# Kernel optimization log

Measured on AMD Instinct MI355X. Metric: run time of the kernel, lower is better.

## Reference

```python
import jax, jax.numpy as jnp
import numpy as np

ALPHA = 0.2  # tf.nn.leaky_relu default alpha
B, LATENT, T, N = 8, 256, 128, 768
F, L, E = 4, 3, 12288


def _causal_conv1d(x, w, b):
    # x: [B,T,Cin], w: [K,Cin,Cout] -> causal pad left by K-1
    k = w.shape[0]
    y = jax.lax.conv_general_dilated(x, w, (1,), ((k - 1, 0),),
                                     dimension_numbers=('NWC', 'WIO', 'NWC'))
    return y + b


def _same_conv1d(x, w, b):
    y = jax.lax.conv_general_dilated(x, w, (1,), 'SAME',
                                     dimension_numbers=('NWC', 'WIO', 'NWC'))
    return y + b


def _same_conv2d(x, w, b):
    y = jax.lax.conv_general_dilated(x, w, (1, 1), 'SAME',
                                     dimension_numbers=('NHWC', 'HWIO', 'NHWC'))
    return y + b


def _gat(nodes, row, col, qw, qb, kw, kb, vw, vb):
    # tf_geometric-style single-head GAT; row/col already contain self-loops.
    M = nodes.shape[0]
    Q = jax.nn.leaky_relu(nodes @ qw + qb, ALPHA)
    K = jax.nn.leaky_relu(nodes @ kw + kb, ALPHA)
    V = nodes @ vw
    scale = jnp.sqrt(jnp.asarray(Q.shape[-1], nodes.dtype))
    score = jnp.sum(Q[row] * K[col], axis=-1) / scale  # [E']
    smax = jax.ops.segment_max(score, row, num_segments=M)
    ex = jnp.exp(score - smax[row])
    den = jax.ops.segment_sum(ex, row, num_segments=M)
    att = ex / den[row]
    out = jax.ops.segment_sum(V[col] * att[:, None], row, num_segments=M)
    return out + vb


def _gw_layer(y, row, col, wa, ba, wb, bb, qw, qb, kw, kb, vw, vb, rw, rb):
    b_, t_, n_, f_ = y.shape
    x = jnp.moveaxis(y, -1, 0)  # [F,B,T,N]

    def branch(xf, wa_, ba_, wb_, bb_, qw_, qb_, kw_, kb_, vw_, vb_):
        a = jax.nn.sigmoid(_causal_conv1d(xf, wa_, ba_))
        g = a * jnp.tanh(_causal_conv1d(xf, wb_, bb_))   # gated TCN [B,T,N]
        nodes = g.transpose(0, 2, 1).reshape(b_ * n_, t_)  # node id = b*N + n
        h = _gat(nodes, row, col, qw_, qb_, kw_, kb_, vw_, vb_)
        return h.reshape(b_, n_, t_).transpose(0, 2, 1)  # [B,T,N]

    outs = jax.vmap(branch)(x, wa, ba, wb, bb, qw, qb, kw, kb, vw, vb)
    outs = jnp.moveaxis(outs, 0, -1)                      # [B,T,N,F]
    res = jnp.einsum('btnf,fg->btng', y, rw) + rb         # 1x1 res conv
    return outs + res


def _decoder(x, edges, shunt_dense_w, shunt_dense_b, shunt_c1_w, shunt_c1_b,
             shunt_c2_w, shunt_c2_b, tcn_a_w, tcn_a_b, tcn_b_w, tcn_b_b,
             gat_q_w, gat_q_b, gat_k_w, gat_k_b, gat_v_w, gat_v_b,
             res_w, res_b, skip_w, skip_b, out1_w, out1_b, out2_w, out2_b):
    # ConvShunt: [B,latent] -> [B,T] -> [B,T,N] -> [B,T,N,F]
    y = x @ shunt_dense_w + shunt_dense_b
    y = _same_conv1d(y[..., None], shunt_c1_w, shunt_c1_b)
    y = _same_conv2d(y[..., None], shunt_c2_w, shunt_c2_b)
    M = B * N
    self_idx = jnp.arange(M, dtype=edges.dtype)
    row = jnp.concatenate([edges[0], self_idx])
    col = jnp.concatenate([edges[1], self_idx])
    skips = []
    for i in range(L):
        y = _gw_layer(y, row, col, tcn_a_w[i], tcn_a_b[i], tcn_b_w[i], tcn_b_b[i],
                      gat_q_w[i], gat_q_b[i], gat_k_w[i], gat_k_b[i],
                      gat_v_w[i], gat_v_b[i], res_w[i], res_b[i])
        skips.append(jax.nn.leaky_relu(
            jnp.einsum('btnf,f->btn', y, skip_w[i]) + skip_b[i], ALPHA))
    s = jnp.stack(skips, axis=-1)                         # [B,T,N,L]
    g = jax.nn.leaky_relu(_same_conv2d(s, out1_w, out1_b), ALPHA)
    return _same_conv2d(g, out2_w, out2_b)                # [B,T,N,1]


def setup_inputs() -> dict:
    ks = iter(jax.random.split(jax.random.key(0), 32))

    def w(shape, fan_in):
        return jax.random.normal(next(ks), shape, jnp.float32) / np.sqrt(fan_in).astype(np.float32)

    return {
        'x': jax.random.normal(next(ks), (B, LATENT), jnp.float32),
        'edges': jax.random.randint(next(ks), (2, E), 0, N, jnp.int32),
        'shunt_dense_w': w((LATENT, T), LATENT),
        'shunt_dense_b': jnp.zeros((T,), jnp.float32),
        'shunt_c1_w': w((3, 1, N), 3),
        'shunt_c1_b': jnp.zeros((N,), jnp.float32),
        'shunt_c2_w': w((3, 3, 1, F), 9),
        'shunt_c2_b': jnp.zeros((F,), jnp.float32),
        'tcn_a_w': w((L, F, 5, N, N), 5 * N),
        'tcn_a_b': jnp.zeros((L, F, N), jnp.float32),
        'tcn_b_w': w((L, F, 5, N, N), 5 * N),
        'tcn_b_b': jnp.zeros((L, F, N), jnp.float32),
        'gat_q_w': w((L, F, T, T), T),
        'gat_q_b': jnp.zeros((L, F, T), jnp.float32),
        'gat_k_w': w((L, F, T, T), T),
        'gat_k_b': jnp.zeros((L, F, T), jnp.float32),
        'gat_v_w': w((L, F, T, T), T),
        'gat_v_b': jnp.zeros((L, F, T), jnp.float32),
        'res_w': w((L, F, F), F),
        'res_b': jnp.zeros((L, F), jnp.float32),
        'skip_w': w((L, F), F),
        'skip_b': jnp.zeros((L,), jnp.float32),
        'out1_w': w((3, 3, L, 1), 9 * L),
        'out1_b': jnp.zeros((1,), jnp.float32),
        'out2_w': w((1, 1, 1, 1), 1),
        'out2_b': jnp.zeros((1,), jnp.float32),
    }


def reference(x, edges, shunt_dense_w, shunt_dense_b, shunt_c1_w, shunt_c1_b,
              shunt_c2_w, shunt_c2_b, tcn_a_w, tcn_a_b, tcn_b_w, tcn_b_b,
              gat_q_w, gat_q_b, gat_k_w, gat_k_b, gat_v_w, gat_v_b,
              res_w, res_b, skip_w, skip_b, out1_w, out1_b, out2_w, out2_b):
    return _decoder(x, edges, shunt_dense_w, shunt_dense_b, shunt_c1_w, shunt_c1_b,
                    shunt_c2_w, shunt_c2_b, tcn_a_w, tcn_a_b, tcn_b_w, tcn_b_b,
                    gat_q_w, gat_q_b, gat_k_w, gat_k_b, gat_v_w, gat_v_b,
                    res_w, res_b, skip_w, skip_b, out1_w, out1_b, out2_w, out2_b)
```

## Files before the change

### kernel.cpp

```cpp
#include <hip/hip_runtime.h>
#include <math.h>

#define ALPHA_ 0.2f
#define AS1 __attribute__((address_space(1)))
#define AS3 __attribute__((address_space(3)))

constexpr int B_ = 8, LATENT_ = 256, T_ = 128, N_ = 768, F_ = 4, L_ = 3, E_ = 12288;
constexpr int M_ = B_ * N_;
constexpr int MT_ = B_ * T_;
constexpr int EP_ = E_ + M_;
constexpr int BTN_ = B_ * T_ * N_;
constexpr size_t SZ_ = (size_t)BTN_ * F_;
constexpr int KTCN_ = 5 * N_;
constexpr int KSPLIT_ = KTCN_ / 2;
constexpr int TP_ = T_ + 4;

typedef __bf16 bf16x8 __attribute__((ext_vector_type(8)));
typedef float f32x4 __attribute__((ext_vector_type(4)));

__device__ __forceinline__ float lrelu(float x) { return x > 0.0f ? x : ALPHA_ * x; }
__device__ __forceinline__ unsigned short f2bf(float x) {
    union { __bf16 h; unsigned short u; } c; c.h = (__bf16)x; return c.u;
}
__device__ __forceinline__ float bf2f(unsigned short u) {
    return __uint_as_float(((unsigned)u) << 16);
}

__global__ void k_dense(const float* __restrict__ x, const float* __restrict__ w,
                        const float* __restrict__ b, float* __restrict__ y0) {
    int i = blockIdx.x * blockDim.x + threadIdx.x;
    if (i >= B_ * T_) return;
    int bb = i / T_, t = i % T_;
    float acc = b[t];
    for (int l = 0; l < LATENT_; ++l) acc += x[bb * LATENT_ + l] * w[l * T_ + t];
    y0[i] = acc;
}

__global__ void k_conv1(const float* __restrict__ y0, const float* __restrict__ w,
                        const float* __restrict__ b, float* __restrict__ y1) {
    int i = blockIdx.x * blockDim.x + threadIdx.x;
    if (i >= BTN_) return;
    int n = i % N_, t = (i / N_) % T_, bb = i / (N_ * T_);
    float acc = b[n];
    #pragma unroll
    for (int k = 0; k < 3; ++k) {
        int tt = t - 1 + k;
        if (tt >= 0 && tt < T_) acc += y0[bb * T_ + tt] * w[k * N_ + n];
    }
    y1[i] = acc;
}

__global__ void k_conv2w(const float* __restrict__ y1, const float* __restrict__ w,
                         const float* __restrict__ b, float* __restrict__ y,
                         unsigned short* __restrict__ xTpad) {
    int i = blockIdx.x * blockDim.x + threadIdx.x;
    if (i >= BTN_) return;
    int n = i % N_, t = (i / N_) % T_, bb = i / (N_ * T_);
    float acc[F_];
    #pragma unroll
    for (int f = 0; f < F_; ++f) acc[f] = b[f];
    #pragma unroll
    for (int dt = 0; dt < 3; ++dt) {
        int tt = t - 1 + dt;
        if (tt < 0 || tt >= T_) continue;
        #pragma unroll
        for (int dn = 0; dn < 3; ++dn) {
            int nn = n - 1 + dn;
            if (nn < 0 || nn >= N_) continue;
            float v = y1[(bb * T_ + tt) * N_ + nn];
            #pragma unroll
            for (int f = 0; f < F_; ++f) acc[f] += v * w[(dt * 3 + dn) * F_ + f];
        }
    }
    #pragma unroll
    for (int f = 0; f < F_; ++f) {
        y[(size_t)i * F_ + f] = acc[f];
        xTpad[((size_t)(f * B_ + bb) * TP_ + 4 + t) * N_ + n] = f2bf(acc[f]);
    }
}

__global__ __launch_bounds__(256) void k_convT(const float* __restrict__ in,
        unsigned short* __restrict__ outT, int Kd, int Nd) {
    __shared__ float tl[32][33];
    const int f = blockIdx.z;
    in += (size_t)f * Kd * Nd;
    outT += (size_t)f * Kd * Nd;
    const int x0 = blockIdx.x * 32;
    const int y0 = blockIdx.y * 32;
    const int tx = threadIdx.x & 31, ty = threadIdx.x >> 5;
    #pragma unroll
    for (int r = 0; r < 4; ++r)
        tl[ty + r * 8][tx] = in[(size_t)(y0 + ty + r * 8) * Nd + x0 + tx];
    __syncthreads();
    #pragma unroll
    for (int r = 0; r < 4; ++r)
        outT[(size_t)(x0 + ty + r * 8) * Kd + y0 + tx] = f2bf(tl[tx][ty + r * 8]);
}

__global__ __launch_bounds__(256) void k_convT2(const float* __restrict__ in0,
        const float* __restrict__ in1, unsigned short* __restrict__ out0,
        unsigned short* __restrict__ out1) {
    __shared__ float tl[64][33];
    const int z = blockIdx.z;
    const int f = z & 3, wsel = z >> 2;
    const float* in = (wsel ? in1 : in0) + (size_t)f * KTCN_ * N_;
    unsigned short* outT = (wsel ? out1 : out0) + (size_t)f * KTCN_ * N_;
    const int n0 = blockIdx.x * 32, k0 = blockIdx.y * 64;
    const int tx = threadIdx.x & 31, ty = threadIdx.x >> 5;
    #pragma unroll
    for (int r = 0; r < 8; ++r)
        tl[ty + r * 8][tx] = in[(size_t)(k0 + ty + r * 8) * N_ + n0 + tx];
    __syncthreads();
    const int kx2 = threadIdx.x & 63, ny = threadIdx.x >> 6;
    #pragma unroll
    for (int r = 0; r < 8; ++r)
        outT[(size_t)(n0 + ny + r * 4) * KTCN_ + k0 + kx2] = f2bf(tl[kx2][ny + r * 4]);
}

__global__ __launch_bounds__(256) void k_tcn_mfma(
        const unsigned short* __restrict__ xTpad,
        const unsigned short* __restrict__ wat, const unsigned short* __restrict__ wbt,
        const float* __restrict__ ba, const float* __restrict__ bbias,
        float* __restrict__ oa0, float* __restrict__ oa1,
        float* __restrict__ ob0, float* __restrict__ ob1) {
    __shared__ unsigned short As[128 * 32];
    __shared__ unsigned short Bs[128 * 32];
    const int bid = blockIdx.x;
    const int bt = bid / 96;
    const int c = bid - bt * 96;
    const int xb = c % 6;
    const int zz = c / 6;
    const int f = zz & 3;
    const int wsel = (zz >> 2) & 1;
    const int s = zz >> 3;
    const int n0 = xb * 128;
    const unsigned short* xf = xTpad + (size_t)(f * B_ + bt) * TP_ * N_;
    const unsigned short* wf = (wsel ? wbt : wat) + (size_t)f * N_ * KTCN_ + (size_t)n0 * KTCN_;
    const float* bias = (wsel ? bbias : ba) + f * N_;
    float* out = (wsel ? (s ? ob1 : ob0) : (s ? oa1 : oa0));
    const int tid = threadIdx.x;
    const int lane = tid & 63;
    const int w = tid >> 6;
    const int wm = (w >> 1) * 64, wn = (w & 1) * 64;
    const int r16 = lane & 15, kb = lane >> 4;
    const int srow = lane >> 2;
    const int scol = (((lane & 3) ^ ((lane >> 3) & 3)) * 8);
    const int kx = (kb ^ ((r16 >> 1) & 3)) * 8;
    f32x4 acc[4][4] = {};
    const int k_lo = s * KSPLIT_, k_hi = k_lo + KSPLIT_;
    for (int kk0 = k_lo; kk0 < k_hi; kk0 += 32) {
        const int ks = kk0 / N_;
        const int nin0 = kk0 - ks * N_;
        #pragma unroll
        for (int h = 0; h < 2; ++h) {
            const int seg = w + 4 * h;
            const int row = seg * 16 + srow;
            const unsigned short* gA = xf + (size_t)(row + ks) * N_ + nin0 + scol;
            const unsigned short* gB = wf + (size_t)row * KTCN_ + kk0 + scol;
            __builtin_amdgcn_global_load_lds((const AS1 unsigned int*)(const void*)gA,
                    (AS3 unsigned int*)(void*)(As + seg * 512), 16, 0, 0);
            __builtin_amdgcn_global_load_lds((const AS1 unsigned int*)(const void*)gB,
                    (AS3 unsigned int*)(void*)(Bs + seg * 512), 16, 0, 0);
        }
        __syncthreads();
        bf16x8 av[4], bv[4];
        #pragma unroll
        for (int i = 0; i < 4; ++i) av[i] = *(const bf16x8*)(As + (wm + i * 16 + r16) * 32 + kx);
        #pragma unroll
        for (int j = 0; j < 4; ++j) bv[j] = *(const bf16x8*)(Bs + (wn + j * 16 + r16) * 32 + kx);
        #pragma unroll
        for (int i = 0; i < 4; ++i)
            #pragma unroll
            for (int j = 0; j < 4; ++j)
                acc[i][j] = __builtin_amdgcn_mfma_f32_16x16x32_bf16(av[i], bv[j], acc[i][j], 0, 0, 0);
        __syncthreads();
    }
    float* of = out + (size_t)(f * B_ + bt) * T_ * N_;
    #pragma unroll
    for (int i = 0; i < 4; ++i) {
        #pragma unroll
        for (int j = 0; j < 4; ++j) {
            const int n = n0 + wn + j * 16 + r16;
            const float bv2 = (s == 0) ? bias[n] : 0.0f;
            #pragma unroll
            for (int r = 0; r < 4; ++r) {
                const int m = wm + i * 16 + kb * 4 + r;
                of[(size_t)m * N_ + n] = acc[i][j][r] + bv2;
            }
        }
    }
}

__global__ __launch_bounds__(256) void k_gate_nodes(const float* __restrict__ a0,
        const float* __restrict__ a1, const float* __restrict__ b0,
        const float* __restrict__ b1, unsigned short* __restrict__ nodes) {
    __shared__ float tl[32][33];
    const int bz = blockIdx.z;
    const int t0 = blockIdx.x * 32, n0 = blockIdx.y * 32;
    const int tx = threadIdx.x & 31, ty = threadIdx.x >> 5;
    const size_t base = (size_t)bz * T_ * N_;
    #pragma unroll
    for (int r = 0; r < 4; ++r) {
        const size_t idx = base + (size_t)(t0 + ty + r * 8) * N_ + n0 + tx;
        const float av = a0[idx] + a1[idx], bvv = b0[idx] + b1[idx];
        tl[ty + r * 8][tx] = (1.0f / (1.0f + __expf(-av))) * tanhf(bvv);
    }
    __syncthreads();
    #pragma unroll
    for (int r = 0; r < 4; ++r)
        nodes[base + (size_t)(n0 + ty + r * 8) * T_ + t0 + tx] = f2bf(tl[tx][ty + r * 8]);
}

__global__ __launch_bounds__(256) void k_proj_mfma(
        const unsigned short* __restrict__ nodes, const unsigned short* __restrict__ pwt,
        const float* __restrict__ qb, const float* __restrict__ kbias,
        unsigned short* __restrict__ Q, unsigned short* __restrict__ K,
        unsigned short* __restrict__ V) {
    __shared__ unsigned short As[128 * 32];
    __shared__ unsigned short Bs[128 * 32];
    const int zz = blockIdx.z;
    const int f = zz & 3;
    const int sel = zz >> 2;
    const int m0 = blockIdx.y * 128;
    const unsigned short* af = nodes + (size_t)f * M_ * T_;
    const unsigned short* wfp = pwt + (size_t)sel * F_ * T_ * T_ + (size_t)f * T_ * T_;
    const float* bias = (sel == 0) ? qb : (sel == 1 ? kbias : nullptr);
    unsigned short* out = (sel == 0) ? Q : (sel == 1 ? K : V);
    const int tid = threadIdx.x;
    const int lane = tid & 63;
    const int w = tid >> 6;
    const int wm = (w >> 1) * 64, wn = (w & 1) * 64;
    const int r16 = lane & 15, kb = lane >> 4;
    const int srow = lane >> 2;
    const int scol = (((lane & 3) ^ ((lane >> 3) & 3)) * 8);
    const int kx = (kb ^ ((r16 >> 1) & 3)) * 8;
    f32x4 acc[4][4] = {};
    for (int kk0 = 0; kk0 < T_; kk0 += 32) {
        #pragma unroll
        for (int h = 0; h < 2; ++h) {
            const int seg = w + 4 * h;
            const int row = seg * 16 + srow;
            const unsigned short* gA = af + (size_t)(m0 + row) * T_ + kk0 + scol;
            const unsigned short* gB = wfp + (size_t)row * T_ + kk0 + scol;
            __builtin_amdgcn_global_load_lds((const AS1 unsigned int*)(const void*)gA,
                    (AS3 unsigned int*)(void*)(As + seg * 512), 16, 0, 0);
            __builtin_amdgcn_global_load_lds((const AS1 unsigned int*)(const void*)gB,
                    (AS3 unsigned int*)(void*)(Bs + seg * 512), 16, 0, 0);
        }
        __syncthreads();
        bf16x8 av[4], bv[4];
        #pragma unroll
        for (int i = 0; i < 4; ++i) av[i] = *(const bf16x8*)(As + (wm + i * 16 + r16) * 32 + kx);
        #pragma unroll
        for (int j = 0; j < 4; ++j) bv[j] = *(const bf16x8*)(Bs + (wn + j * 16 + r16) * 32 + kx);
        #pragma unroll
        for (int i = 0; i < 4; ++i)
            #pragma unroll
            for (int j = 0; j < 4; ++j)
                acc[i][j] = __builtin_amdgcn_mfma_f32_16x16x32_bf16(av[i], bv[j], acc[i][j], 0, 0, 0);
        __syncthreads();
    }
    const int do_l = (sel < 2);
    unsigned short* of = out + (size_t)f * M_ * T_;
    #pragma unroll
    for (int i = 0; i < 4; ++i) {
        #pragma unroll
        for (int j = 0; j < 4; ++j) {
            const int n = wn + j * 16 + r16;
            #pragma unroll
            for (int r = 0; r < 4; ++r) {
                const int m = m0 + wm + i * 16 + kb * 4 + r;
                float v = acc[i][j][r];
                if (bias) v += bias[f * T_ + n];
                if (do_l) v = lrelu(v);
                of[(size_t)m * T_ + n] = f2bf(v);
            }
        }
    }
}

__device__ __forceinline__ int edge_row(const int* e, int i) { return i < E_ ? e[i] : i - E_; }
__device__ __forceinline__ int edge_col(const int* e, int i) { return i < E_ ? e[E_ + i] : i - E_; }

__global__ void k_hist(const int* __restrict__ edges, int* __restrict__ deg) {
    int i = blockIdx.x * blockDim.x + threadIdx.x;
    if (i >= EP_) return;
    atomicAdd(&deg[edge_row(edges, i)], 1);
}

__global__ __launch_bounds__(256) void k_scan(const int* __restrict__ deg,
        int* __restrict__ rowptr, int* __restrict__ cursor) {
    __shared__ int part[256];
    const int tid = threadIdx.x;
    constexpr int PER = M_ / 256;
    int loc[PER];
    int s = 0;
    #pragma unroll
    for (int j = 0; j < PER; ++j) { loc[j] = s; s += deg[tid * PER + j]; }
    part[tid] = s;
    __syncthreads();
    if (tid == 0) {
        int run = 0;
        for (int i2 = 0; i2 < 256; ++i2) { int v = part[i2]; part[i2] = run; run += v; }
        rowptr[M_] = run;
    }
    __syncthreads();
    const int off = part[tid];
    #pragma unroll
    for (int j = 0; j < PER; ++j) {
        rowptr[tid * PER + j] = off + loc[j];
        cursor[tid * PER + j] = off + loc[j];
    }
}

__global__ void k_scatter(const int* __restrict__ edges, int* __restrict__ cursor,
                          int* __restrict__ csr_col) {
    int i = blockIdx.x * blockDim.x + threadIdx.x;
    if (i >= EP_) return;
    int r = edge_row(edges, i), c = edge_col(edges, i);
    int pos = atomicAdd(&cursor[r], 1);
    csr_col[pos] = c;
}

__global__ __launch_bounds__(256) void k_gat(const unsigned short* __restrict__ Q,
        const unsigned short* __restrict__ Kb, const unsigned short* __restrict__ V,
        const int* __restrict__ rowptr, const int* __restrict__ csr_col,
        float* __restrict__ H) {
    constexpr int CAP = 128;
    __shared__ float sc[4][CAP];
    const int w = threadIdx.x >> 6, lane = threadIdx.x & 63;
    const int wv = blockIdx.x * 4 + w;
    const int f = wv / M_, r = wv - f * M_;
    const int p0 = rowptr[r], p1 = rowptr[r + 1];
    const unsigned short* Qr = Q + ((size_t)f * M_ + r) * T_;
    const float q0 = bf2f(Qr[lane]), q1 = bf2f(Qr[lane + 64]);
    float mx = -3.4e38f;
    for (int j = p0; j < p1; ++j) {
        const unsigned short* Kc = Kb + ((size_t)f * M_ + csr_col[j]) * T_;
        float s = q0 * bf2f(Kc[lane]) + q1 * bf2f(Kc[lane + 64]);
        #pragma unroll
        for (int mk = 32; mk >= 1; mk >>= 1) s += __shfl_xor(s, mk);
        s *= 0.0883883476483184f;
        if (lane == 0 && j - p0 < CAP) sc[w][j - p0] = s;
        mx = fmaxf(mx, s);
    }
    float den = 0.0f;
    for (int j = p0; j < p1; ++j) {
        float s;
        if (j - p0 < CAP) s = sc[w][j - p0];
        else {
            const unsigned short* Kc = Kb + ((size_t)f * M_ + csr_col[j]) * T_;
            s = q0 * bf2f(Kc[lane]) + q1 * bf2f(Kc[lane + 64]);
            #pragma unroll
            for (int mk = 32; mk >= 1; mk >>= 1) s += __shfl_xor(s, mk);
            s *= 0.0883883476483184f;
        }
        den += __expf(s - mx);
    }
    const float rden = 1.0f / den;
    float a0 = 0.0f, a1 = 0.0f;
    for (int j = p0; j < p1; ++j) {
        const int c = csr_col[j];
        float s;
        if (j - p0 < CAP) s = sc[w][j - p0];
        else {
            const unsigned short* Kc = Kb + ((size_t)f * M_ + c) * T_;
            s = q0 * bf2f(Kc[lane]) + q1 * bf2f(Kc[lane + 64]);
            #pragma unroll
            for (int mk = 32; mk >= 1; mk >>= 1) s += __shfl_xor(s, mk);
            s *= 0.0883883476483184f;
        }
        const float att = __expf(s - mx) * rden;
        const unsigned short* Vc = V + ((size_t)f * M_ + c) * T_;
        a0 += att * bf2f(Vc[lane]);
        a1 += att * bf2f(Vc[lane + 64]);
    }
    float* Hr = H + ((size_t)f * M_ + r) * T_;
    Hr[lane] = a0;
    Hr[lane + 64] = a1;
}

__global__ __launch_bounds__(256) void k_combine_t(const float* __restrict__ y,
        const float* __restrict__ H, const float* __restrict__ vb,
        const float* __restrict__ rw, const float* __restrict__ rb,
        const float* __restrict__ skw, const float* __restrict__ skb, int layer,
        float* __restrict__ ynext, unsigned short* __restrict__ xTpad,
        float* __restrict__ sbufp) {
    __shared__ float hl[F_][32][33];
    const int b = blockIdx.z;
    const int t0 = blockIdx.x * 32, n0 = blockIdx.y * 32;
    const int tx = threadIdx.x & 31, ty = threadIdx.x >> 5;
    #pragma unroll
    for (int g = 0; g < F_; ++g)
        #pragma unroll
        for (int r = 0; r < 4; ++r) {
            const int nn = ty + r * 8;
            hl[g][nn][tx] = H[((size_t)g * M_ + b * N_ + n0 + nn) * T_ + t0 + tx];
        }
    __syncthreads();
    #pragma unroll
    for (int r = 0; r < 4; ++r) {
        const int tt = ty + r * 8;
        const int t = t0 + tt;
        const size_t i = ((size_t)b * T_ + t) * N_ + n0 + tx;
        const float4 y4 = *(const float4*)(y + i * 4);
        float o[F_];
        #pragma unroll
        for (int g = 0; g < F_; ++g) {
            float acc = hl[g][tx][tt] + vb[g * T_ + t] + rb[g];
            acc += y4.x * rw[0 * F_ + g] + y4.y * rw[1 * F_ + g]
                 + y4.z * rw[2 * F_ + g] + y4.w * rw[3 * F_ + g];
            o[g] = acc;
        }
        float4 o4 = {o[0], o[1], o[2], o[3]};
        *(float4*)(ynext + i * 4) = o4;
        #pragma unroll
        for (int g = 0; g < F_; ++g)
            xTpad[((size_t)(g * B_ + b) * TP_ + 4 + t) * N_ + n0 + tx] = f2bf(o[g]);
        float sk = skb[layer];
        #pragma unroll
        for (int g = 0; g < F_; ++g) sk += o[g] * skw[layer * F_ + g];
        sbufp[(size_t)layer * BTN_ + i] = lrelu(sk);
    }
}

__global__ void k_final(const float* __restrict__ sbufp, const float* __restrict__ o1w,
        const float* __restrict__ o1b, const float* __restrict__ o2w,
        const float* __restrict__ o2b, float* __restrict__ out) {
    int i = blockIdx.x * blockDim.x + threadIdx.x;
    if (i >= BTN_) return;
    int n = i % N_, t = (i / N_) % T_, bb = i / (N_ * T_);
    float acc = o1b[0];
    #pragma unroll
    for (int dt = 0; dt < 3; ++dt) {
        int tt = t - 1 + dt;
        if (tt < 0 || tt >= T_) continue;
        #pragma unroll
        for (int dn = 0; dn < 3; ++dn) {
            int nn = n - 1 + dn;
            if (nn < 0 || nn >= N_) continue;
            const size_t base = (size_t)(bb * T_ + tt) * N_ + nn;
            #pragma unroll
            for (int l = 0; l < L_; ++l)
                acc += sbufp[(size_t)l * BTN_ + base] * o1w[(dt * 3 + dn) * L_ + l];
        }
    }
    float g = lrelu(acc);
    out[i] = g * o2w[0] + o2b[0];
}

extern "C" void kernel_launch(void* const* d_in, const int* in_sizes, int n_in,
                              void* d_out, int out_size, void* d_ws, size_t ws_size,
                              hipStream_t stream) {
    const float* x       = (const float*)d_in[0];
    const int*   edges   = (const int*)d_in[1];
    const float* sd_w    = (const float*)d_in[2];
    const float* sd_b    = (const float*)d_in[3];
    const float* c1w     = (const float*)d_in[4];
    const float* c1b     = (const float*)d_in[5];
    const float* c2w     = (const float*)d_in[6];
    const float* c2b     = (const float*)d_in[7];
    const float* tcn_a_w = (const float*)d_in[8];
    const float* tcn_a_b = (const float*)d_in[9];
    const float* tcn_b_w = (const float*)d_in[10];
    const float* tcn_b_b = (const float*)d_in[11];
    const float* gat_q_w = (const float*)d_in[12];
    const float* gat_q_b = (const float*)d_in[13];
    const float* gat_k_w = (const float*)d_in[14];
    const float* gat_k_b = (const float*)d_in[15];
    const float* gat_v_w = (const float*)d_in[16];
    const float* gat_v_b = (const float*)d_in[17];
    const float* res_w   = (const float*)d_in[18];
    const float* res_b   = (const float*)d_in[19];
    const float* skip_w  = (const float*)d_in[20];
    const float* skip_b  = (const float*)d_in[21];
    const float* out1_w  = (const float*)d_in[22];
    const float* out1_b  = (const float*)d_in[23];
    const float* out2_w  = (const float*)d_in[24];
    const float* out2_b  = (const float*)d_in[25];
    float* out = (float*)d_out;

    float* ws = (float*)d_ws;
    size_t off = 0;
    auto alloc = [&](size_t nf) { float* p = ws + off; off += nf; return p; };
    float* ybuf  = alloc(SZ_);
    float* y2buf = alloc(SZ_);
    float* H     = alloc(SZ_);
    float* apre  = alloc(SZ_);
    float* bpre  = alloc(SZ_);
    float* V     = alloc(SZ_);
    float* sbufp = alloc((size_t)BTN_ * L_);
    float* y0    = alloc(MT_);
    float* y1    = alloc(BTN_);
    unsigned short* xTpad  = (unsigned short*)alloc((size_t)F_ * B_ * TP_ * N_ / 2 + 16);
    unsigned short* nodesb = (unsigned short*)alloc(SZ_ / 2);
    unsigned short* qb16   = (unsigned short*)alloc(SZ_ / 2);
    unsigned short* kb16   = (unsigned short*)alloc(SZ_ / 2);
    unsigned short* vb16   = (unsigned short*)alloc(SZ_ / 2);
    unsigned short* wat = (unsigned short*)alloc((size_t)F_ * KTCN_ * N_ / 2);
    unsigned short* wbt = (unsigned short*)alloc((size_t)F_ * KTCN_ * N_ / 2);
    unsigned short* pwt = (unsigned short*)alloc((size_t)3 * F_ * T_ * T_ / 2);
    int* rowptr  = (int*)alloc(M_ + 1);
    int* cursor  = (int*)alloc(M_);
    int* deg     = (int*)alloc(M_);
    int* csr_col = (int*)alloc(EP_);
    (void)ws_size; (void)in_sizes; (void)n_in; (void)out_size;

    hipMemsetAsync(xTpad, 0, (size_t)F_ * B_ * TP_ * N_ * 2, stream);
    hipMemsetAsync(deg, 0, M_ * 4, stream);
    k_hist<<<(EP_ + 255) / 256, 256, 0, stream>>>(edges, deg);
    k_scan<<<1, 256, 0, stream>>>(deg, rowptr, cursor);
    k_scatter<<<(EP_ + 255) / 256, 256, 0, stream>>>(edges, cursor, csr_col);

    k_dense<<<(B_ * T_ + 255) / 256, 256, 0, stream>>>(x, sd_w, sd_b, y0);
    k_conv1<<<(BTN_ + 255) / 256, 256, 0, stream>>>(y0, c1w, c1b, y1);
    k_conv2w<<<(BTN_ + 255) / 256, 256, 0, stream>>>(y1, c2w, c2b, ybuf, xTpad);

    float* cur = ybuf;
    float* nxt = y2buf;
    for (int layer = 0; layer < L_; ++layer) {
        const float* wa = tcn_a_w + (size_t)layer * F_ * KTCN_ * N_;
        const float* ba = tcn_a_b + (size_t)layer * F_ * N_;
        const float* wb = tcn_b_w + (size_t)layer * F_ * KTCN_ * N_;
        const float* bb = tcn_b_b + (size_t)layer * F_ * N_;
        const float* qw = gat_q_w + (size_t)layer * F_ * T_ * T_;
        const float* qb = gat_q_b + (size_t)layer * F_ * T_;
        const float* kw = gat_k_w + (size_t)layer * F_ * T_ * T_;
        const float* kbias = gat_k_b + (size_t)layer * F_ * T_;
        const float* vw = gat_v_w + (size_t)layer * F_ * T_ * T_;
        const float* vb = gat_v_b + (size_t)layer * F_ * T_;
        const float* rw = res_w + (size_t)layer * F_ * F_;
        const float* rb = res_b + (size_t)layer * F_;

        dim3 gw2(N_ / 32, KTCN_ / 64, 2 * F_);
        k_convT2<<<gw2, 256, 0, stream>>>(wa, wb, wat, wbt);
        k_tcn_mfma<<<768, 256, 0, stream>>>(xTpad, wat, wbt, ba, bb, apre, V, bpre, H);
        dim3 gg(T_ / 32, N_ / 32, F_ * B_);
        k_gate_nodes<<<gg, 256, 0, stream>>>(apre, V, bpre, H, nodesb);
        dim3 gpw(T_ / 32, T_ / 32, F_);
        const int PWOFF = F_ * T_ * T_;
        k_convT<<<gpw, 256, 0, stream>>>(qw, pwt, T_, T_);
        k_convT<<<gpw, 256, 0, stream>>>(kw, pwt + PWOFF, T_, T_);
        k_convT<<<gpw, 256, 0, stream>>>(vw, pwt + 2 * PWOFF, T_, T_);
        dim3 gp(1, M_ / 128, 12);
        k_proj_mfma<<<gp, 256, 0, stream>>>(nodesb, pwt, qb, kbias, qb16, kb16, vb16);
        k_gat<<<(F_ * M_) / 4, 256, 0, stream>>>(qb16, kb16, vb16, rowptr, csr_col, H);
        dim3 gc(T_ / 32, N_ / 32, B_);
        k_combine_t<<<gc, 256, 0, stream>>>(cur, H, vb, rw, rb, skip_w, skip_b,
                layer, nxt, xTpad, sbufp);
        float* tmp = cur; cur = nxt; nxt = tmp;
    }
    k_final<<<(BTN_ + 255) / 256, 256, 0, stream>>>(sbufp, out1_w, out1_b, out2_w, out2_b, out);
}
```

Measured before the change: 584.6 us.

## Store TCN split-K partials and GAT output in bf16; batch weight transposes

The split-K TCN partial outputs and the GAT output H are now stored as bf16 rather than fp32, which halves their write and read traffic in the gate and combine kernels. The per-layer weight transposes for the TCN and the Q/K/V projections are merged into two launches before the layer loop, covering all layers at once. This removes many small launches and cuts intermediate bandwidth. In exchange it adds bf16 rounding to the pre-activations and attention output, and it needs a larger workspace to hold the transposed weights for every layer.

```diff
diff --git a/kernel.cpp b/kernel.cpp
--- a/kernel.cpp
+++ b/kernel.cpp
@@ -79,32 +79,15 @@
     }
 }
 
-__global__ __launch_bounds__(256) void k_convT(const float* __restrict__ in,
-        unsigned short* __restrict__ outT, int Kd, int Nd) {
-    __shared__ float tl[32][33];
-    const int f = blockIdx.z;
-    in += (size_t)f * Kd * Nd;
-    outT += (size_t)f * Kd * Nd;
-    const int x0 = blockIdx.x * 32;
-    const int y0 = blockIdx.y * 32;
-    const int tx = threadIdx.x & 31, ty = threadIdx.x >> 5;
-    #pragma unroll
-    for (int r = 0; r < 4; ++r)
-        tl[ty + r * 8][tx] = in[(size_t)(y0 + ty + r * 8) * Nd + x0 + tx];
-    __syncthreads();
-    #pragma unroll
-    for (int r = 0; r < 4; ++r)
-        outT[(size_t)(x0 + ty + r * 8) * Kd + y0 + tx] = f2bf(tl[tx][ty + r * 8]);
-}
-
-__global__ __launch_bounds__(256) void k_convT2(const float* __restrict__ in0,
-        const float* __restrict__ in1, unsigned short* __restrict__ out0,
-        unsigned short* __restrict__ out1) {
+__global__ __launch_bounds__(256) void k_convT2(const float* __restrict__ aw,
+        const float* __restrict__ bw, unsigned short* __restrict__ wat3,
+        unsigned short* __restrict__ wbt3) {
     __shared__ float tl[64][33];
     const int z = blockIdx.z;
-    const int f = z & 3, wsel = z >> 2;
-    const float* in = (wsel ? in1 : in0) + (size_t)f * KTCN_ * N_;
-    unsigned short* outT = (wsel ? out1 : out0) + (size_t)f * KTCN_ * N_;
+    const int f = z & 3, wsel = (z >> 2) & 1, layer = z >> 3;
+    const size_t toff = ((size_t)layer * F_ + f) * KTCN_ * N_;
+    const float* in = (wsel ? bw : aw) + toff;
+    unsigned short* outT = (wsel ? wbt3 : wat3) + toff;
     const int n0 = blockIdx.x * 32, k0 = blockIdx.y * 64;
     const int tx = threadIdx.x & 31, ty = threadIdx.x >> 5;
     #pragma unroll
@@ -117,12 +100,35 @@
         outT[(size_t)(n0 + ny + r * 4) * KTCN_ + k0 + kx2] = f2bf(tl[kx2][ny + r * 4]);
 }
 
+__global__ __launch_bounds__(256) void k_convTproj(const float* __restrict__ qw,
+        const float* __restrict__ kw, const float* __restrict__ vw,
+        unsigned short* __restrict__ pwt3) {
+    __shared__ float tl[32][33];
+    const int z = blockIdx.z;
+    const int f = z & 3;
+    const int sel = (z >> 2) % 3;
+    const int layer = z / 12;
+    const float* in = (sel == 0 ? qw : (sel == 1 ? kw : vw))
+                      + ((size_t)layer * F_ + f) * T_ * T_;
+    unsigned short* outT = pwt3 + (((size_t)layer * 3 + sel) * F_ + f) * T_ * T_;
+    const int x0 = blockIdx.x * 32;
+    const int y0 = blockIdx.y * 32;
+    const int tx = threadIdx.x & 31, ty = threadIdx.x >> 5;
+    #pragma unroll
+    for (int r = 0; r < 4; ++r)
+        tl[ty + r * 8][tx] = in[(size_t)(y0 + ty + r * 8) * T_ + x0 + tx];
+    __syncthreads();
+    #pragma unroll
+    for (int r = 0; r < 4; ++r)
+        outT[(size_t)(x0 + ty + r * 8) * T_ + y0 + tx] = f2bf(tl[tx][ty + r * 8]);
+}
+
 __global__ __launch_bounds__(256) void k_tcn_mfma(
         const unsigned short* __restrict__ xTpad,
         const unsigned short* __restrict__ wat, const unsigned short* __restrict__ wbt,
         const float* __restrict__ ba, const float* __restrict__ bbias,
-        float* __restrict__ oa0, float* __restrict__ oa1,
-        float* __restrict__ ob0, float* __restrict__ ob1) {
+        unsigned short* __restrict__ oa0, unsigned short* __restrict__ oa1,
+        unsigned short* __restrict__ ob0, unsigned short* __restrict__ ob1) {
     __shared__ unsigned short As[128 * 32];
     __shared__ unsigned short Bs[128 * 32];
     const int bid = blockIdx.x;
@@ -137,7 +143,7 @@
     const unsigned short* xf = xTpad + (size_t)(f * B_ + bt) * TP_ * N_;
     const unsigned short* wf = (wsel ? wbt : wat) + (size_t)f * N_ * KTCN_ + (size_t)n0 * KTCN_;
     const float* bias = (wsel ? bbias : ba) + f * N_;
-    float* out = (wsel ? (s ? ob1 : ob0) : (s ? oa1 : oa0));
+    unsigned short* out = (wsel ? (s ? ob1 : ob0) : (s ? oa1 : oa0));
     const int tid = threadIdx.x;
     const int lane = tid & 63;
     const int w = tid >> 6;
@@ -175,7 +181,7 @@
                 acc[i][j] = __builtin_amdgcn_mfma_f32_16x16x32_bf16(av[i], bv[j], acc[i][j], 0, 0, 0);
         __syncthreads();
     }
-    float* of = out + (size_t)(f * B_ + bt) * T_ * N_;
+    unsigned short* of = out + (size_t)(f * B_ + bt) * T_ * N_;
     #pragma unroll
     for (int i = 0; i < 4; ++i) {
         #pragma unroll
@@ -185,15 +191,15 @@
             #pragma unroll
             for (int r = 0; r < 4; ++r) {
                 const int m = wm + i * 16 + kb * 4 + r;
-                of[(size_t)m * N_ + n] = acc[i][j][r] + bv2;
+                of[(size_t)m * N_ + n] = f2bf(acc[i][j][r] + bv2);
             }
         }
     }
 }
 
-__global__ __launch_bounds__(256) void k_gate_nodes(const float* __restrict__ a0,
-        const float* __restrict__ a1, const float* __restrict__ b0,
-        const float* __restrict__ b1, unsigned short* __restrict__ nodes) {
+__global__ __launch_bounds__(256) void k_gate_nodes(const unsigned short* __restrict__ a0,
+        const unsigned short* __restrict__ a1, const unsigned short* __restrict__ b0,
+        const unsigned short* __restrict__ b1, unsigned short* __restrict__ nodes) {
     __shared__ float tl[32][33];
     const int bz = blockIdx.z;
     const int t0 = blockIdx.x * 32, n0 = blockIdx.y * 32;
@@ -202,7 +208,8 @@
     #pragma unroll
     for (int r = 0; r < 4; ++r) {
         const size_t idx = base + (size_t)(t0 + ty + r * 8) * N_ + n0 + tx;
-        const float av = a0[idx] + a1[idx], bvv = b0[idx] + b1[idx];
+        const float av = bf2f(a0[idx]) + bf2f(a1[idx]);
+        const float bvv = bf2f(b0[idx]) + bf2f(b1[idx]);
         tl[ty + r * 8][tx] = (1.0f / (1.0f + __expf(-av))) * tanhf(bvv);
     }
     __syncthreads();
@@ -325,7 +332,7 @@
 __global__ __launch_bounds__(256) void k_gat(const unsigned short* __restrict__ Q,
         const unsigned short* __restrict__ Kb, const unsigned short* __restrict__ V,
         const int* __restrict__ rowptr, const int* __restrict__ csr_col,
-        float* __restrict__ H) {
+        unsigned short* __restrict__ H) {
     constexpr int CAP = 128;
     __shared__ float sc[4][CAP];
     const int w = threadIdx.x >> 6, lane = threadIdx.x & 63;
@@ -375,13 +382,13 @@
         a0 += att * bf2f(Vc[lane]);
         a1 += att * bf2f(Vc[lane + 64]);
     }
-    float* Hr = H + ((size_t)f * M_ + r) * T_;
-    Hr[lane] = a0;
-    Hr[lane + 64] = a1;
+    unsigned short* Hr = H + ((size_t)f * M_ + r) * T_;
+    Hr[lane] = f2bf(a0);
+    Hr[lane + 64] = f2bf(a1);
 }
 
 __global__ __launch_bounds__(256) void k_combine_t(const float* __restrict__ y,
-        const float* __restrict__ H, const float* __restrict__ vb,
+        const unsigned short* __restrict__ H, const float* __restrict__ vb,
         const float* __restrict__ rw, const float* __restrict__ rb,
         const float* __restrict__ skw, const float* __restrict__ skb, int layer,
         float* __restrict__ ynext, unsigned short* __restrict__ xTpad,
@@ -395,7 +402,7 @@
         #pragma unroll
         for (int r = 0; r < 4; ++r) {
             const int nn = ty + r * 8;
-            hl[g][nn][tx] = H[((size_t)g * M_ + b * N_ + n0 + nn) * T_ + t0 + tx];
+            hl[g][nn][tx] = bf2f(H[((size_t)g * M_ + b * N_ + n0 + nn) * T_ + t0 + tx]);
         }
     __syncthreads();
     #pragma unroll
@@ -485,10 +492,6 @@
     auto alloc = [&](size_t nf) { float* p = ws + off; off += nf; return p; };
     float* ybuf  = alloc(SZ_);
     float* y2buf = alloc(SZ_);
-    float* H     = alloc(SZ_);
-    float* apre  = alloc(SZ_);
-    float* bpre  = alloc(SZ_);
-    float* V     = alloc(SZ_);
     float* sbufp = alloc((size_t)BTN_ * L_);
     float* y0    = alloc(MT_);
     float* y1    = alloc(BTN_);
@@ -497,9 +500,14 @@
     unsigned short* qb16   = (unsigned short*)alloc(SZ_ / 2);
     unsigned short* kb16   = (unsigned short*)alloc(SZ_ / 2);
     unsigned short* vb16   = (unsigned short*)alloc(SZ_ / 2);
-    unsigned short* wat = (unsigned short*)alloc((size_t)F_ * KTCN_ * N_ / 2);
-    unsigned short* wbt = (unsigned short*)alloc((size_t)F_ * KTCN_ * N_ / 2);
-    unsigned short* pwt = (unsigned short*)alloc((size_t)3 * F_ * T_ * T_ / 2);
+    unsigned short* Hb     = (unsigned short*)alloc(SZ_ / 2);
+    unsigned short* pa0    = (unsigned short*)alloc(SZ_ / 2);
+    unsigned short* pa1    = (unsigned short*)alloc(SZ_ / 2);
+    unsigned short* pb0    = (unsigned short*)alloc(SZ_ / 2);
+    unsigned short* pb1    = (unsigned short*)alloc(SZ_ / 2);
+    unsigned short* wat3 = (unsigned short*)alloc((size_t)L_ * F_ * KTCN_ * N_ / 2);
+    unsigned short* wbt3 = (unsigned short*)alloc((size_t)L_ * F_ * KTCN_ * N_ / 2);
+    unsigned short* pwt3 = (unsigned short*)alloc((size_t)L_ * 3 * F_ * T_ * T_ / 2);
     int* rowptr  = (int*)alloc(M_ + 1);
     int* cursor  = (int*)alloc(M_);
     int* deg     = (int*)alloc(M_);
@@ -512,6 +520,11 @@
     k_scan<<<1, 256, 0, stream>>>(deg, rowptr, cursor);
     k_scatter<<<(EP_ + 255) / 256, 256, 0, stream>>>(edges, cursor, csr_col);
 
+    dim3 gw2(N_ / 32, KTCN_ / 64, 8 * L_);
+    k_convT2<<<gw2, 256, 0, stream>>>(tcn_a_w, tcn_b_w, wat3, wbt3);
+    dim3 gpw(T_ / 32, T_ / 32, 12 * L_);
+    k_convTproj<<<gpw, 256, 0, stream>>>(gat_q_w, gat_k_w, gat_v_w, pwt3);
+
     k_dense<<<(B_ * T_ + 255) / 256, 256, 0, stream>>>(x, sd_w, sd_b, y0);
     k_conv1<<<(BTN_ + 255) / 256, 256, 0, stream>>>(y0, c1w, c1b, y1);
     k_conv2w<<<(BTN_ + 255) / 256, 256, 0, stream>>>(y1, c2w, c2b, ybuf, xTpad);
@@ -519,34 +532,25 @@
     float* cur = ybuf;
     float* nxt = y2buf;
     for (int layer = 0; layer < L_; ++layer) {
-        const float* wa = tcn_a_w + (size_t)layer * F_ * KTCN_ * N_;
         const float* ba = tcn_a_b + (size_t)layer * F_ * N_;
-        const float* wb = tcn_b_w + (size_t)layer * F_ * KTCN_ * N_;
         const float* bb = tcn_b_b + (size_t)layer * F_ * N_;
-        const float* qw = gat_q_w + (size_t)layer * F_ * T_ * T_;
         const float* qb = gat_q_b + (size_t)layer * F_ * T_;
-        const float* kw = gat_k_w + (size_t)layer * F_ * T_ * T_;
         const float* kbias = gat_k_b + (size_t)layer * F_ * T_;
-        const float* vw = gat_v_w + (size_t)layer * F_ * T_ * T_;
         const float* vb = gat_v_b + (size_t)layer * F_ * T_;
         const float* rw = res_w + (size_t)layer * F_ * F_;
         const float* rb = res_b + (size_t)layer * F_;
-
-        dim3 gw2(N_ / 32, KTCN_ / 64, 2 * F_);
-        k_convT2<<<gw2, 256, 0, stream>>>(wa, wb, wat, wbt);
-        k_tcn_mfma<<<768, 256, 0, stream>>>(xTpad, wat, wbt, ba, bb, apre, V, bpre, H);
+        const unsigned short* wat = wat3 + (size_t)layer * F_ * KTCN_ * N_;
+        const unsigned short* wbt = wbt3 + (size_t)layer * F_ * KTCN_ * N_;
+        const unsigned short* pwt = pwt3 + (size_t)layer * 3 * F_ * T_ * T_;
+
+        k_tcn_mfma<<<768, 256, 0, stream>>>(xTpad, wat, wbt, ba, bb, pa0, pa1, pb0, pb1);
         dim3 gg(T_ / 32, N_ / 32, F_ * B_);
-        k_gate_nodes<<<gg, 256, 0, stream>>>(apre, V, bpre, H, nodesb);
-        dim3 gpw(T_ / 32, T_ / 32, F_);
-        const int PWOFF = F_ * T_ * T_;
-        k_convT<<<gpw, 256, 0, stream>>>(qw, pwt, T_, T_);
-        k_convT<<<gpw, 256, 0, stream>>>(kw, pwt + PWOFF, T_, T_);
-        k_convT<<<gpw, 256, 0, stream>>>(vw, pwt + 2 * PWOFF, T_, T_);
+        k_gate_nodes<<<gg, 256, 0, stream>>>(pa0, pa1, pb0, pb1, nodesb);
         dim3 gp(1, M_ / 128, 12);
         k_proj_mfma<<<gp, 256, 0, stream>>>(nodesb, pwt, qb, kbias, qb16, kb16, vb16);
-        k_gat<<<(F_ * M_) / 4, 256, 0, stream>>>(qb16, kb16, vb16, rowptr, csr_col, H);
+        k_gat<<<(F_ * M_) / 4, 256, 0, stream>>>(qb16, kb16, vb16, rowptr, csr_col, Hb);
         dim3 gc(T_ / 32, N_ / 32, B_);
-        k_combine_t<<<gc, 256, 0, stream>>>(cur, H, vb, rw, rb, skip_w, skip_b,
+        k_combine_t<<<gc, 256, 0, stream>>>(cur, Hb, vb, rw, rb, skip_w, skip_b,
                 layer, nxt, xTpad, sbufp);
         float* tmp = cur; cur = nxt; nxt = tmp;
     }
```

Result: no change. 577.5 us (-1.2%).
